# Kernel tuning notes

Measured on AMD Instinct MI355X. Metric: run time of the kernel, lower is better.

Reference implementation:

```python
import jax, jax.numpy as jnp
import numpy as np

HASH_BUCKETS = 1000
EMB_DIM = 16
LSTM_UNITS = 32
DENSE_UNITS = 32


def setup_inputs() -> dict:
    key = jax.random.key(0)
    ks = jax.random.split(key, 8)
    B, T = 4096, 512
    ids = jax.random.randint(ks[0], (B, T), 0, HASH_BUCKETS, dtype=jnp.int32)
    emb = jax.random.normal(ks[1], (HASH_BUCKETS, EMB_DIM), jnp.float32) * 0.05
    kernel = jax.random.normal(ks[2], (EMB_DIM, 4 * LSTM_UNITS), jnp.float32) * 0.1
    rec_kernel = jax.random.normal(ks[3], (LSTM_UNITS, 4 * LSTM_UNITS), jnp.float32) * 0.1
    w1 = jax.random.normal(ks[4], (LSTM_UNITS, DENSE_UNITS), jnp.float32) * 0.1
    b1 = jnp.zeros((DENSE_UNITS,), jnp.float32)
    w2 = jax.random.normal(ks[5], (DENSE_UNITS, 1), jnp.float32) * 0.1
    b2 = jnp.zeros((1,), jnp.float32)
    return {"ids": ids, "emb": emb, "kernel": kernel, "rec_kernel": rec_kernel,
            "w1": w1, "b1": b1, "w2": w2, "b2": b2}


def _lstm(x, kernel, rec_kernel):
    # x: [B, T, E]; Keras LSTM, use_bias=False, return last hidden state [B, H]
    B = x.shape[0]
    H = rec_kernel.shape[0]
    # precompute input projections for all timesteps: [T, B, 4H]
    xz = jnp.einsum('bte,ef->tbf', x, kernel)

    def step(carry, xz_t):
        h, c = carry
        z = xz_t + h @ rec_kernel  # [B, 4H]
        zi, zf, zc, zo = jnp.split(z, 4, axis=-1)  # Keras gate order i,f,c,o
        i = jax.nn.sigmoid(zi)
        f = jax.nn.sigmoid(zf)
        c = f * c + i * jnp.tanh(zc)
        o = jax.nn.sigmoid(zo)
        h = o * jnp.tanh(c)
        return (h, c), None

    init = (jnp.zeros((B, H), x.dtype), jnp.zeros((B, H), x.dtype))
    (h, _), _ = jax.lax.scan(step, init, xz)
    return h


def reference(ids, emb, kernel, rec_kernel, w1, b1, w2, b2):
    x = emb[ids]                        # [B, T, E] embedding lookup
    h = _lstm(x, kernel, rec_kernel)    # [B, H]
    y = jax.nn.relu(h @ w1 + b1)        # [B, 32]
    return y @ w2 + b2                  # [B, 1]
```

## Files before the change

### kernel.cpp

```cpp
#include <hip/hip_runtime.h>
#include <stdint.h>

#define HASH_BUCKETS 1000
#define EMB_DIM 16
#define HDIM 32
#define G4 128
#define TSTEPS 512
#define BATCH 4096

typedef short v8s __attribute__((ext_vector_type(8)));
typedef float v4f __attribute__((ext_vector_type(4)));

__device__ __forceinline__ float frcp(float x) {
    float r; asm("v_rcp_f32 %0, %1" : "=v"(r) : "v"(x)); return r;
}
__device__ __forceinline__ float fexp2(float x) {
    float r; asm("v_exp_f32 %0, %1" : "=v"(r) : "v"(x)); return r;
}
__device__ __forceinline__ uint32_t cvtpk_bf16(float lo, float hi) {
    uint32_t r; asm("v_cvt_pk_bf16_f32 %0, %1, %2" : "=v"(r) : "v"(lo), "v"(hi)); return r;
}
__device__ __forceinline__ uint32_t bf16rne(float x) {
    uint32_t u = __float_as_uint(x);
    return (u + 0x7FFFu + ((u >> 16) & 1u)) >> 16;
}

__global__ void precompute_P2_kernel(const float* __restrict__ emb,
                                     const float* __restrict__ kern,
                                     float* __restrict__ P2) {
    int idx = blockIdx.x * blockDim.x + threadIdx.x;
    if (idx >= HASH_BUCKETS * G4) return;
    int row = idx >> 7;
    int c2  = idx & 127;
    int h = c2 >> 2;
    int g = c2 & 3;
    float acc = 0.f;
#pragma unroll
    for (int e = 0; e < EMB_DIM; ++e)
        acc = fmaf(emb[row * EMB_DIM + e], kern[e * G4 + g * 32 + h], acc);
    float sg = (g == 2) ? 2.8853900817779268f : -1.4426950408889634f;
    P2[idx] = acc * sg;
}

__global__ __launch_bounds__(256)
__attribute__((amdgpu_waves_per_eu(1, 1)))
void lstm_head_kernel(const int* __restrict__ ids,
                      const float* __restrict__ P2,
                      const float* __restrict__ R,
                      const float* __restrict__ w1,
                      const float* __restrict__ b1,
                      const float* __restrict__ w2,
                      const float* __restrict__ b2,
                      float* __restrict__ out) {
    __shared__ __align__(16) uint32_t hbuf[2][16][36];
    __shared__ float hfin[16][33];

    const int tid  = threadIdx.x;
    const int w    = tid >> 6;
    const int lane = tid & 63;
    const int col  = lane & 15;
    const int quad = lane >> 4;
    const int bb   = blockIdx.x * 16;
    const int h0   = 8 * w + quad;
    const int h1   = h0 + 4;
    const int sw   = col & 3;

    const float PL2E   =  2.8853900817779268f;
    const float N2PL2E = -5.7707801635558536f;

    union V8 { uint32_t u[4]; v8s v; };
    V8 A0hi, A0lo, A1hi, A1lo;
    {
        int tt = col >> 2, g = col & 3;
        float sg = (g == 2) ? PL2E : -1.4426950408889634f;
        int gc0 = g * 32 + 8 * w + tt;
        int gc1 = gc0 + 4;
#pragma unroll
        for (int r = 0; r < 4; ++r) {
            uint32_t h0p[2], l0p[2], h1p[2], l1p[2];
#pragma unroll
            for (int e = 0; e < 2; ++e) {
                int k = quad * 8 + r + 4 * e;
                float x0 = R[k * G4 + gc0] * sg;
                uint32_t hb0 = bf16rne(x0);
                h0p[e] = hb0;
                l0p[e] = bf16rne(x0 - __uint_as_float(hb0 << 16));
                float x1 = R[k * G4 + gc1] * sg;
                uint32_t hb1 = bf16rne(x1);
                h1p[e] = hb1;
                l1p[e] = bf16rne(x1 - __uint_as_float(hb1 << 16));
            }
            A0hi.u[r] = h0p[0] | (h0p[1] << 16);
            A0lo.u[r] = l0p[0] | (l0p[1] << 16);
            A1hi.u[r] = h1p[0] | (h1p[1] << 16);
            A1lo.u[r] = l1p[0] | (l1p[1] << 16);
        }
    }

    for (int i = tid; i < 2 * 16 * 36; i += 256)
        ((uint32_t*)hbuf)[i] = 0u;

    const int* __restrict__ idrow = ids + (size_t)(bb + col) * TSTEPS;
    int ida = idrow[0];
    float4 xz0_c = *(const float4*)(P2 + (size_t)ida * G4 + 4 * h0);
    float4 xz1_c = *(const float4*)(P2 + (size_t)ida * G4 + 4 * h1);
    int idb = idrow[1];
    float4 xz0_n = *(const float4*)(P2 + (size_t)idb * G4 + 4 * h0);
    float4 xz1_n = *(const float4*)(P2 + (size_t)idb * G4 + 4 * h1);
    int id_c = idrow[2];
    int id_n = idrow[3];

    float c0 = 0.f, c1 = 0.f, hv0 = 0.f, hv1 = 0.f;
    const v4f vzero = {0.f, 0.f, 0.f, 0.f};

    const uint32_t* rdp[2] = { &hbuf[0][col][8 * (quad ^ sw)],
                               &hbuf[1][col][8 * (quad ^ sw)] };
    uint32_t* wrp[2] = { &hbuf[1][col][8 * (w ^ sw) + 2 * quad],
                         &hbuf[0][col][8 * (w ^ sw) + 2 * quad] };

    __syncthreads();

#define STEP(PB, T)                                                             \
    {                                                                           \
                  \
        uint4 dA = *(const uint4*)(rdp[PB]);                                    \
        uint4 dB = *(const uint4*)(rdp[PB] + 4);                                \
                      \
        float4 xz0_f = *(const float4*)(P2 + (size_t)id_c * G4 + 4 * h0);       \
        float4 xz1_f = *(const float4*)(P2 + (size_t)id_c * G4 + 4 * h1);       \
        int id_f = idrow[((T) + 4 < TSTEPS) ? ((T) + 4) : (TSTEPS - 1)];        \
        V8 Bhi, Blo;                                                            \
        Bhi.u[0] = __builtin_amdgcn_perm(dA.y, dA.x, 0x07060302u);              \
        Bhi.u[1] = __builtin_amdgcn_perm(dA.w, dA.z, 0x07060302u);              \
        Bhi.u[2] = __builtin_amdgcn_perm(dB.y, dB.x, 0x07060302u);              \
        Bhi.u[3] = __builtin_amdgcn_perm(dB.w, dB.z, 0x07060302u);              \
        Blo.u[0] = __builtin_amdgcn_perm(dA.y, dA.x, 0x05040100u);              \
        Blo.u[1] = __builtin_amdgcn_perm(dA.w, dA.z, 0x05040100u);              \
        Blo.u[2] = __builtin_amdgcn_perm(dB.y, dB.x, 0x05040100u);              \
        Blo.u[3] = __builtin_amdgcn_perm(dB.w, dB.z, 0x05040100u);              \
        v4f xzv0 = {xz0_c.x, xz0_c.y, xz0_c.z, xz0_c.w};                        \
        v4f xzv1 = {xz1_c.x, xz1_c.y, xz1_c.z, xz1_c.w};                        \
           \
        v4f m0a = __builtin_amdgcn_mfma_f32_16x16x32_bf16(A0lo.v, Bhi.v, vzero, 0, 0, 0); \
        v4f m0b = __builtin_amdgcn_mfma_f32_16x16x32_bf16(A0hi.v, Blo.v, vzero, 0, 0, 0); \
        v4f m0c = __builtin_amdgcn_mfma_f32_16x16x32_bf16(A0hi.v, Bhi.v, xzv0, 0, 0, 0);  \
        v4f m1a = __builtin_amdgcn_mfma_f32_16x16x32_bf16(A1lo.v, Bhi.v, vzero, 0, 0, 0); \
        v4f m1b = __builtin_amdgcn_mfma_f32_16x16x32_bf16(A1hi.v, Blo.v, vzero, 0, 0, 0); \
        v4f m1c = __builtin_amdgcn_mfma_f32_16x16x32_bf16(A1hi.v, Bhi.v, xzv1, 0, 0, 0);  \
        v4f z0 = (m0a + m0b) + m0c;                                             \
        v4f z1 = (m1a + m1b) + m1c;                                             \
                         \
        float di0 = 1.f + fexp2(z0[0]);                                         \
        float df0 = 1.f + fexp2(z0[1]);                                         \
        float dc0 = 1.f + fexp2(z0[2]);                                         \
        float dq0 = 1.f + fexp2(z0[3]);                                         \
        float di1 = 1.f + fexp2(z1[0]);                                         \
        float df1 = 1.f + fexp2(z1[1]);                                         \
        float dc1 = 1.f + fexp2(z1[2]);                                         \
        float dq1 = 1.f + fexp2(z1[3]);                                         \
        float Pp0 = di0 * df0, Qq0 = dc0 * dq0;                                 \
        float Pp1 = di1 * df1, Qq1 = dc1 * dq1;                                 \
        float rr0 = frcp(Pp0 * Qq0);                                            \
        float rr1 = frcp(Pp1 * Qq1);                                            \
        float rP0 = rr0 * Qq0, rQ0 = rr0 * Pp0;                                 \
        float rP1 = rr1 * Qq1, rQ1 = rr1 * Pp1;                                 \
        float ig0 = rP0 * df0, fg0 = rP0 * di0, rc0 = rQ0 * dq0, og0 = rQ0 * dc0; \
        float ig1 = rP1 * df1, fg1 = rP1 * di1, rc1 = rQ1 * dq1, og1 = rQ1 * dc1; \
        float tz0 = fmaf(N2PL2E, rc0, PL2E);                 \
        float tz1 = fmaf(N2PL2E, rc1, PL2E);                                    \
        c0 = fmaf(fg0, c0, ig0 * tz0);        \
        c1 = fmaf(fg1, c1, ig1 * tz1);                                          \
        float tc0 = fmaf(-2.f, frcp(1.f + fexp2(c0)), 1.f);                     \
        float tc1 = fmaf(-2.f, frcp(1.f + fexp2(c1)), 1.f);                     \
        hv0 = og0 * tc0;                                                        \
        hv1 = og1 * tc1;                                                        \
              \
        uint32_t t0 = cvtpk_bf16(hv0, hv0);                                     \
        float lo0 = hv0 - __uint_as_float(t0 & 0xffff0000u);                    \
        uint32_t pk0 = cvtpk_bf16(lo0, hv0);                                    \
        uint32_t t1 = cvtpk_bf16(hv1, hv1);                                     \
        float lo1 = hv1 - __uint_as_float(t1 & 0xffff0000u);                    \
        uint32_t pk1 = cvtpk_bf16(lo1, hv1);                                    \
        uint2 wv; wv.x = pk0; wv.y = pk1;                                       \
        *(uint2*)(wrp[PB]) = wv;   \
        xz0_c = xz0_n; xz1_c = xz1_n;                                           \
        xz0_n = xz0_f; xz1_n = xz1_f;                                           \
        id_c = id_n; id_n = id_f;                                               \
                                  \
        asm volatile("s_waitcnt lgkmcnt(0)\n\ts_barrier" ::: "memory");         \
    }

    for (int t = 0; t < TSTEPS; t += 2) {
        STEP(0, t)
        STEP(1, t + 1)
    }
#undef STEP

    hfin[col][h0] = hv0;
    hfin[col][h1] = hv1;
    __syncthreads();

    int u = tid & 31;
    for (int bq = tid >> 5; bq < 16; bq += 8) {
        float y = b1[u];
#pragma unroll
        for (int k = 0; k < HDIM; ++k)
            y = fmaf(hfin[bq][k], w1[k * HDIM + u], y);
        y = fmaxf(y, 0.f);
        float vv = y * w2[u];
#pragma unroll
        for (int off = 16; off >= 1; off >>= 1)
            vv += __shfl_xor(vv, off);
        if (u == 0) out[bb + bq] = vv + b2[0];
    }
}

extern "C" void kernel_launch(void* const* d_in, const int* in_sizes, int n_in,
                              void* d_out, int out_size, void* d_ws, size_t ws_size,
                              hipStream_t stream) {
    const int*   ids  = (const int*)d_in[0];
    const float* emb  = (const float*)d_in[1];
    const float* kern = (const float*)d_in[2];
    const float* rec  = (const float*)d_in[3];
    const float* w1   = (const float*)d_in[4];
    const float* b1   = (const float*)d_in[5];
    const float* w2   = (const float*)d_in[6];
    const float* b2   = (const float*)d_in[7];
    float* out = (float*)d_out;
    float* P2  = (float*)d_ws;

    precompute_P2_kernel<<<(HASH_BUCKETS * G4 + 255) / 256, 256, 0, stream>>>(
        emb, kern, P2);
    lstm_head_kernel<<<BATCH / 16, 256, 0, stream>>>(
        ids, P2, rec, w1, b1, w2, b2, out);
}
```

Baseline: 298.0 us.

## Split LSTM hidden units across eight waves with one unit per lane

Doubles the workgroup from 4 to 8 waves, so each lane computes one hidden unit instead of two. This halves the MFMA work and gate math per wave on the serial recurrence. The shared hidden-state buffer now stores separate hi/lo bf16 planes written as 16-bit stores, which removes the perm unpacking before the MFMA, and the swizzle and row stride change to match. In exchange, the per-step barrier now synchronizes 8 waves and the kernel allows 2 waves per EU. The extra sub-word stores may add LDS traffic.

```diff
diff --git a/kernel.cpp b/kernel.cpp
--- a/kernel.cpp
+++ b/kernel.cpp
@@ -7,6 +7,7 @@
 #define G4 128
 #define TSTEPS 512
 #define BATCH 4096
+#define RSTRIDE 40
 
 typedef short v8s __attribute__((ext_vector_type(8)));
 typedef float v4f __attribute__((ext_vector_type(4)));
@@ -17,8 +18,8 @@
 __device__ __forceinline__ float fexp2(float x) {
     float r; asm("v_exp_f32 %0, %1" : "=v"(r) : "v"(x)); return r;
 }
-__device__ __forceinline__ uint32_t cvtpk_bf16(float lo, float hi) {
-    uint32_t r; asm("v_cvt_pk_bf16_f32 %0, %1, %2" : "=v"(r) : "v"(lo), "v"(hi)); return r;
+__device__ __forceinline__ uint32_t cvtpk_bf16(float a, float b) {
+    uint32_t r; asm("v_cvt_pk_bf16_f32 %0, %1, %2" : "=v"(r) : "v"(a), "v"(b)); return r;
 }
 __device__ __forceinline__ uint32_t bf16rne(float x) {
     uint32_t u = __float_as_uint(x);
@@ -42,8 +43,8 @@
     P2[idx] = acc * sg;
 }
 
-__global__ __launch_bounds__(256)
-__attribute__((amdgpu_waves_per_eu(1, 1)))
+__global__ __launch_bounds__(512)
+__attribute__((amdgpu_waves_per_eu(2)))
 void lstm_head_kernel(const int* __restrict__ ids,
                       const float* __restrict__ P2,
                       const float* __restrict__ R,
@@ -52,7 +53,7 @@
                       const float* __restrict__ w2,
                       const float* __restrict__ b2,
                       float* __restrict__ out) {
-    __shared__ __align__(16) uint32_t hbuf[2][16][36];
+    __shared__ __align__(16) uint32_t hbuf[2][16][RSTRIDE];
     __shared__ float hfin[16][33];
 
     const int tid  = threadIdx.x;
@@ -61,132 +62,101 @@
     const int col  = lane & 15;
     const int quad = lane >> 4;
     const int bb   = blockIdx.x * 16;
-    const int h0   = 8 * w + quad;
-    const int h1   = h0 + 4;
-    const int sw   = col & 3;
+    const int unit = 4 * w + quad;
+    const int sw   = (col ^ (col >> 2)) & 3;
 
     const float PL2E   =  2.8853900817779268f;
+    const float NL2E   = -1.4426950408889634f;
     const float N2PL2E = -5.7707801635558536f;
 
     union V8 { uint32_t u[4]; v8s v; };
-    V8 A0hi, A0lo, A1hi, A1lo;
+    V8 Ahi, Alo;
     {
         int tt = col >> 2, g = col & 3;
-        float sg = (g == 2) ? PL2E : -1.4426950408889634f;
-        int gc0 = g * 32 + 8 * w + tt;
-        int gc1 = gc0 + 4;
+        float sg = (g == 2) ? PL2E : NL2E;
+        int gc = g * 32 + 4 * w + tt;
 #pragma unroll
         for (int r = 0; r < 4; ++r) {
-            uint32_t h0p[2], l0p[2], h1p[2], l1p[2];
+            uint32_t hp[2], lp[2];
 #pragma unroll
             for (int e = 0; e < 2; ++e) {
                 int k = quad * 8 + r + 4 * e;
-                float x0 = R[k * G4 + gc0] * sg;
-                uint32_t hb0 = bf16rne(x0);
-                h0p[e] = hb0;
-                l0p[e] = bf16rne(x0 - __uint_as_float(hb0 << 16));
-                float x1 = R[k * G4 + gc1] * sg;
-                uint32_t hb1 = bf16rne(x1);
-                h1p[e] = hb1;
-                l1p[e] = bf16rne(x1 - __uint_as_float(hb1 << 16));
+                float x = R[k * G4 + gc] * sg;
+                uint32_t hb = bf16rne(x);
+                hp[e] = hb;
+                lp[e] = bf16rne(x - __uint_as_float(hb << 16));
             }
-            A0hi.u[r] = h0p[0] | (h0p[1] << 16);
-            A0lo.u[r] = l0p[0] | (l0p[1] << 16);
-            A1hi.u[r] = h1p[0] | (h1p[1] << 16);
-            A1lo.u[r] = l1p[0] | (l1p[1] << 16);
+            Ahi.u[r] = hp[0] | (hp[1] << 16);
+            Alo.u[r] = lp[0] | (lp[1] << 16);
         }
     }
 
-    for (int i = tid; i < 2 * 16 * 36; i += 256)
+    for (int i = tid; i < 2 * 16 * RSTRIDE; i += 512)
         ((uint32_t*)hbuf)[i] = 0u;
+
+    const uint32_t* rdH[2] = { &hbuf[0][col][4 * (quad ^ sw)],
+                               &hbuf[1][col][4 * (quad ^ sw)] };
+    uint16_t* base16 = (uint16_t*)&hbuf[0][0][0];
+    const int bufhalf = 16 * RSTRIDE * 2;
+    {
+    }
+    const int hidw = col * RSTRIDE + 4 * (((w >> 1)) ^ sw) + quad;
+    const int h16  = hidw * 2 + (w & 1);
+    const int l16  = h16 + 32;
+    uint16_t* wrH[2] = { base16 + bufhalf + h16, base16 + h16 };
+    uint16_t* wrL[2] = { base16 + bufhalf + l16, base16 + l16 };
 
     const int* __restrict__ idrow = ids + (size_t)(bb + col) * TSTEPS;
     int ida = idrow[0];
-    float4 xz0_c = *(const float4*)(P2 + (size_t)ida * G4 + 4 * h0);
-    float4 xz1_c = *(const float4*)(P2 + (size_t)ida * G4 + 4 * h1);
+    float4 xz_c = *(const float4*)(P2 + (size_t)ida * G4 + 4 * unit);
     int idb = idrow[1];
-    float4 xz0_n = *(const float4*)(P2 + (size_t)idb * G4 + 4 * h0);
-    float4 xz1_n = *(const float4*)(P2 + (size_t)idb * G4 + 4 * h1);
+    float4 xz_n = *(const float4*)(P2 + (size_t)idb * G4 + 4 * unit);
     int id_c = idrow[2];
     int id_n = idrow[3];
 
-    float c0 = 0.f, c1 = 0.f, hv0 = 0.f, hv1 = 0.f;
+    float cc = 0.f, hv = 0.f;
     const v4f vzero = {0.f, 0.f, 0.f, 0.f};
 
-    const uint32_t* rdp[2] = { &hbuf[0][col][8 * (quad ^ sw)],
-                               &hbuf[1][col][8 * (quad ^ sw)] };
-    uint32_t* wrp[2] = { &hbuf[1][col][8 * (w ^ sw) + 2 * quad],
-                         &hbuf[0][col][8 * (w ^ sw) + 2 * quad] };
-
     __syncthreads();
+
+    union V8R { uint4 q; v8s v; };
 
 #define STEP(PB, T)                                                             \
     {                                                                           \
-                  \
-        uint4 dA = *(const uint4*)(rdp[PB]);                                    \
-        uint4 dB = *(const uint4*)(rdp[PB] + 4);                                \
-                      \
-        float4 xz0_f = *(const float4*)(P2 + (size_t)id_c * G4 + 4 * h0);       \
-        float4 xz1_f = *(const float4*)(P2 + (size_t)id_c * G4 + 4 * h1);       \
+                                  \
+        V8R Bhi, Blo;                                                           \
+        Bhi.q = *(const uint4*)(rdH[PB]);                                       \
+        Blo.q = *(const uint4*)(rdH[PB] + 16);                                  \
+                     \
+        float4 xz_f = *(const float4*)(P2 + (size_t)id_c * G4 + 4 * unit);      \
         int id_f = idrow[((T) + 4 < TSTEPS) ? ((T) + 4) : (TSTEPS - 1)];        \
-        V8 Bhi, Blo;                                                            \
-        Bhi.u[0] = __builtin_amdgcn_perm(dA.y, dA.x, 0x07060302u);              \
-        Bhi.u[1] = __builtin_amdgcn_perm(dA.w, dA.z, 0x07060302u);              \
-        Bhi.u[2] = __builtin_amdgcn_perm(dB.y, dB.x, 0x07060302u);              \
-        Bhi.u[3] = __builtin_amdgcn_perm(dB.w, dB.z, 0x07060302u);              \
-        Blo.u[0] = __builtin_amdgcn_perm(dA.y, dA.x, 0x05040100u);              \
-        Blo.u[1] = __builtin_amdgcn_perm(dA.w, dA.z, 0x05040100u);              \
-        Blo.u[2] = __builtin_amdgcn_perm(dB.y, dB.x, 0x05040100u);              \
-        Blo.u[3] = __builtin_amdgcn_perm(dB.w, dB.z, 0x05040100u);              \
-        v4f xzv0 = {xz0_c.x, xz0_c.y, xz0_c.z, xz0_c.w};                        \
-        v4f xzv1 = {xz1_c.x, xz1_c.y, xz1_c.z, xz1_c.w};                        \
-           \
-        v4f m0a = __builtin_amdgcn_mfma_f32_16x16x32_bf16(A0lo.v, Bhi.v, vzero, 0, 0, 0); \
-        v4f m0b = __builtin_amdgcn_mfma_f32_16x16x32_bf16(A0hi.v, Blo.v, vzero, 0, 0, 0); \
-        v4f m0c = __builtin_amdgcn_mfma_f32_16x16x32_bf16(A0hi.v, Bhi.v, xzv0, 0, 0, 0);  \
-        v4f m1a = __builtin_amdgcn_mfma_f32_16x16x32_bf16(A1lo.v, Bhi.v, vzero, 0, 0, 0); \
-        v4f m1b = __builtin_amdgcn_mfma_f32_16x16x32_bf16(A1hi.v, Blo.v, vzero, 0, 0, 0); \
-        v4f m1c = __builtin_amdgcn_mfma_f32_16x16x32_bf16(A1hi.v, Bhi.v, xzv1, 0, 0, 0);  \
-        v4f z0 = (m0a + m0b) + m0c;                                             \
-        v4f z1 = (m1a + m1b) + m1c;                                             \
-                         \
-        float di0 = 1.f + fexp2(z0[0]);                                         \
-        float df0 = 1.f + fexp2(z0[1]);                                         \
-        float dc0 = 1.f + fexp2(z0[2]);                                         \
-        float dq0 = 1.f + fexp2(z0[3]);                                         \
-        float di1 = 1.f + fexp2(z1[0]);                                         \
-        float df1 = 1.f + fexp2(z1[1]);                                         \
-        float dc1 = 1.f + fexp2(z1[2]);                                         \
-        float dq1 = 1.f + fexp2(z1[3]);                                         \
-        float Pp0 = di0 * df0, Qq0 = dc0 * dq0;                                 \
-        float Pp1 = di1 * df1, Qq1 = dc1 * dq1;                                 \
-        float rr0 = frcp(Pp0 * Qq0);                                            \
-        float rr1 = frcp(Pp1 * Qq1);                                            \
-        float rP0 = rr0 * Qq0, rQ0 = rr0 * Pp0;                                 \
-        float rP1 = rr1 * Qq1, rQ1 = rr1 * Pp1;                                 \
-        float ig0 = rP0 * df0, fg0 = rP0 * di0, rc0 = rQ0 * dq0, og0 = rQ0 * dc0; \
-        float ig1 = rP1 * df1, fg1 = rP1 * di1, rc1 = rQ1 * dq1, og1 = rQ1 * dc1; \
-        float tz0 = fmaf(N2PL2E, rc0, PL2E);                 \
-        float tz1 = fmaf(N2PL2E, rc1, PL2E);                                    \
-        c0 = fmaf(fg0, c0, ig0 * tz0);        \
-        c1 = fmaf(fg1, c1, ig1 * tz1);                                          \
-        float tc0 = fmaf(-2.f, frcp(1.f + fexp2(c0)), 1.f);                     \
-        float tc1 = fmaf(-2.f, frcp(1.f + fexp2(c1)), 1.f);                     \
-        hv0 = og0 * tc0;                                                        \
-        hv1 = og1 * tc1;                                                        \
-              \
-        uint32_t t0 = cvtpk_bf16(hv0, hv0);                                     \
-        float lo0 = hv0 - __uint_as_float(t0 & 0xffff0000u);                    \
-        uint32_t pk0 = cvtpk_bf16(lo0, hv0);                                    \
-        uint32_t t1 = cvtpk_bf16(hv1, hv1);                                     \
-        float lo1 = hv1 - __uint_as_float(t1 & 0xffff0000u);                    \
-        uint32_t pk1 = cvtpk_bf16(lo1, hv1);                                    \
-        uint2 wv; wv.x = pk0; wv.y = pk1;                                       \
-        *(uint2*)(wrp[PB]) = wv;   \
-        xz0_c = xz0_n; xz1_c = xz1_n;                                           \
-        xz0_n = xz0_f; xz1_n = xz1_f;                                           \
+        v4f xzv = {xz_c.x, xz_c.y, xz_c.z, xz_c.w};                             \
+        v4f ma = __builtin_amdgcn_mfma_f32_16x16x32_bf16(Alo.v, Bhi.v, vzero, 0, 0, 0); \
+        v4f mb = __builtin_amdgcn_mfma_f32_16x16x32_bf16(Ahi.v, Blo.v, vzero, 0, 0, 0); \
+        v4f mc = __builtin_amdgcn_mfma_f32_16x16x32_bf16(Ahi.v, Bhi.v, xzv, 0, 0, 0);   \
+        v4f z = (ma + mb) + mc;                                                 \
+                                               \
+        float di = 1.f + fexp2(z[0]);                                           \
+        float df = 1.f + fexp2(z[1]);                                           \
+        float dc = 1.f + fexp2(z[2]);                                           \
+        float dq = 1.f + fexp2(z[3]);                                           \
+        float Pp = di * df, Qq = dc * dq;                                       \
+        float rr = frcp(Pp * Qq);                                               \
+        float rP = rr * Qq, rQ = rr * Pp;                                       \
+        float ig = rP * df, fg = rP * di, rc = rQ * dq, og = rQ * dc;           \
+        float tz = fmaf(N2PL2E, rc, PL2E);                   \
+        cc = fmaf(fg, cc, ig * tz);                \
+        float tc = fmaf(-2.f, frcp(1.f + fexp2(cc)), 1.f);                      \
+        hv = og * tc;                                                           \
+                               \
+        uint32_t th = cvtpk_bf16(hv, hv);                                       \
+        wrH[PB][0] = (uint16_t)th;                                              \
+        float lo = hv - __uint_as_float(th << 16);                              \
+        uint32_t tl = cvtpk_bf16(lo, lo);                                       \
+        wrL[PB][0] = (uint16_t)tl;                                              \
+        xz_c = xz_n; xz_n = xz_f;                                               \
         id_c = id_n; id_n = id_f;                                               \
-                                  \
+                                               \
         asm volatile("s_waitcnt lgkmcnt(0)\n\ts_barrier" ::: "memory");         \
     }
 
@@ -196,12 +166,12 @@
     }
 #undef STEP
 
-    hfin[col][h0] = hv0;
-    hfin[col][h1] = hv1;
+    hfin[col][unit] = hv;
     __syncthreads();
 
-    int u = tid & 31;
-    for (int bq = tid >> 5; bq < 16; bq += 8) {
+    int u  = tid & 31;
+    int bq = tid >> 5;
+    {
         float y = b1[u];
 #pragma unroll
         for (int k = 0; k < HDIM; ++k)
@@ -231,6 +201,6 @@
 
     precompute_P2_kernel<<<(HASH_BUCKETS * G4 + 255) / 256, 256, 0, stream>>>(
         emb, kern, P2);
-    lstm_head_kernel<<<BATCH / 16, 256, 0, stream>>>(
+    lstm_head_kernel<<<BATCH / 16, 512, 0, stream>>>(
         ids, P2, rec, w1, b1, w2, b2, out);
 }
```

New measurement: 299.4 us. No clear change (+0.5%).

## Store hidden state as separate hi/lo bf16 planes to drop per-step permutes

Applied to the files above, without the earlier changes.

Changes the hidden-unit-to-lane mapping so each lane owns adjacent units, and writes the bf16 hi and lo parts of h into separate shared-memory planes. MFMA B operands then load directly without v_perm repacking, and one cvt_pk converts two units at once. The xz prefetch is restructured into even/odd register sets, and the P2 loads are moved to after the MFMA issue so they overlap. The XOR swizzle is removed, which may bring back LDS bank conflicts.

```diff
diff --git a/kernel.cpp b/kernel.cpp
--- a/kernel.cpp
+++ b/kernel.cpp
@@ -17,8 +17,8 @@
 __device__ __forceinline__ float fexp2(float x) {
     float r; asm("v_exp_f32 %0, %1" : "=v"(r) : "v"(x)); return r;
 }
-__device__ __forceinline__ uint32_t cvtpk_bf16(float lo, float hi) {
-    uint32_t r; asm("v_cvt_pk_bf16_f32 %0, %1, %2" : "=v"(r) : "v"(lo), "v"(hi)); return r;
+__device__ __forceinline__ uint32_t cvtpk_bf16(float a, float b) {
+    uint32_t r; asm("v_cvt_pk_bf16_f32 %0, %1, %2" : "=v"(r) : "v"(a), "v"(b)); return r;
 }
 __device__ __forceinline__ uint32_t bf16rne(float x) {
     uint32_t u = __float_as_uint(x);
@@ -61,26 +61,26 @@
     const int col  = lane & 15;
     const int quad = lane >> 4;
     const int bb   = blockIdx.x * 16;
-    const int h0   = 8 * w + quad;
-    const int h1   = h0 + 4;
-    const int sw   = col & 3;
+    const int u0   = 8 * w + 2 * quad;
+    const int u1   = u0 + 1;
 
     const float PL2E   =  2.8853900817779268f;
+    const float NL2E   = -1.4426950408889634f;
     const float N2PL2E = -5.7707801635558536f;
 
     union V8 { uint32_t u[4]; v8s v; };
     V8 A0hi, A0lo, A1hi, A1lo;
     {
         int tt = col >> 2, g = col & 3;
-        float sg = (g == 2) ? PL2E : -1.4426950408889634f;
-        int gc0 = g * 32 + 8 * w + tt;
-        int gc1 = gc0 + 4;
+        float sg = (g == 2) ? PL2E : NL2E;
+        int gc0 = g * 32 + 8 * w + 2 * tt;
+        int gc1 = gc0 + 1;
 #pragma unroll
         for (int r = 0; r < 4; ++r) {
             uint32_t h0p[2], l0p[2], h1p[2], l1p[2];
 #pragma unroll
             for (int e = 0; e < 2; ++e) {
-                int k = quad * 8 + r + 4 * e;
+                int k = quad * 8 + 2 * r + e;
                 float x0 = R[k * G4 + gc0] * sg;
                 uint32_t hb0 = bf16rne(x0);
                 h0p[e] = hb0;
@@ -100,56 +100,54 @@
     for (int i = tid; i < 2 * 16 * 36; i += 256)
         ((uint32_t*)hbuf)[i] = 0u;
 
+    const uint32_t* rd[2] = { &hbuf[0][col][4 * quad],
+                              &hbuf[1][col][4 * quad] };
+    uint32_t* wr[2] = { &hbuf[1][col][4 * w + quad],
+                        &hbuf[0][col][4 * w + quad] };
+
     const int* __restrict__ idrow = ids + (size_t)(bb + col) * TSTEPS;
-    int ida = idrow[0];
-    float4 xz0_c = *(const float4*)(P2 + (size_t)ida * G4 + 4 * h0);
-    float4 xz1_c = *(const float4*)(P2 + (size_t)ida * G4 + 4 * h1);
-    int idb = idrow[1];
-    float4 xz0_n = *(const float4*)(P2 + (size_t)idb * G4 + 4 * h0);
-    float4 xz1_n = *(const float4*)(P2 + (size_t)idb * G4 + 4 * h1);
-    int id_c = idrow[2];
-    int id_n = idrow[3];
+    const float* __restrict__ baseL = P2 + 4 * u0;
+    v4f xzE0, xzE1, xzO0, xzO1;
+    {
+        const float* p0 = baseL + (size_t)idrow[0] * G4;
+        const float* p1 = baseL + (size_t)idrow[1] * G4;
+        xzE0 = *(const v4f*)(p0);
+        xzE1 = *(const v4f*)(p0 + 4);
+        xzO0 = *(const v4f*)(p1);
+        xzO1 = *(const v4f*)(p1 + 4);
+    }
+    int idE = idrow[2];
+    int idO = idrow[3];
 
     float c0 = 0.f, c1 = 0.f, hv0 = 0.f, hv1 = 0.f;
     const v4f vzero = {0.f, 0.f, 0.f, 0.f};
 
-    const uint32_t* rdp[2] = { &hbuf[0][col][8 * (quad ^ sw)],
-                               &hbuf[1][col][8 * (quad ^ sw)] };
-    uint32_t* wrp[2] = { &hbuf[1][col][8 * (w ^ sw) + 2 * quad],
-                         &hbuf[0][col][8 * (w ^ sw) + 2 * quad] };
-
     __syncthreads();
 
-#define STEP(PB, T)                                                             \
+    union V8R { uint4 q; v8s v; };
+
+#define STEP(PB, XZ0, XZ1, IDX, T)                                              \
     {                                                                           \
-                  \
-        uint4 dA = *(const uint4*)(rdp[PB]);                                    \
-        uint4 dB = *(const uint4*)(rdp[PB] + 4);                                \
+             \
+        V8R Bhi, Blo;                                                           \
+        Bhi.q = *(const uint4*)(rd[PB]);                                        \
+        Blo.q = *(const uint4*)(rd[PB] + 16);                                   \
+        v4f ma0 = __builtin_amdgcn_mfma_f32_16x16x32_bf16(A0lo.v, Bhi.v, vzero, 0, 0, 0); \
+        v4f mb0 = __builtin_amdgcn_mfma_f32_16x16x32_bf16(A0hi.v, Blo.v, vzero, 0, 0, 0); \
+        v4f mc0 = __builtin_amdgcn_mfma_f32_16x16x32_bf16(A0hi.v, Bhi.v, XZ0, 0, 0, 0);   \
+        v4f ma1 = __builtin_amdgcn_mfma_f32_16x16x32_bf16(A1lo.v, Bhi.v, vzero, 0, 0, 0); \
+        v4f mb1 = __builtin_amdgcn_mfma_f32_16x16x32_bf16(A1hi.v, Blo.v, vzero, 0, 0, 0); \
+        v4f mc1 = __builtin_amdgcn_mfma_f32_16x16x32_bf16(A1hi.v, Bhi.v, XZ1, 0, 0, 0);   \
+            \
+        {                                                                       \
+            const float* pf_ = baseL + (size_t)(IDX) * G4;                      \
+            XZ0 = *(const v4f*)(pf_);                                           \
+            XZ1 = *(const v4f*)(pf_ + 4);                                       \
+        }                                                                       \
+        { int nt_ = (T) + 4; IDX = idrow[nt_ < TSTEPS ? nt_ : (TSTEPS - 1)]; }  \
+        v4f z0 = (ma0 + mb0) + mc0;                                             \
+        v4f z1 = (ma1 + mb1) + mc1;                                             \
                       \
-        float4 xz0_f = *(const float4*)(P2 + (size_t)id_c * G4 + 4 * h0);       \
-        float4 xz1_f = *(const float4*)(P2 + (size_t)id_c * G4 + 4 * h1);       \
-        int id_f = idrow[((T) + 4 < TSTEPS) ? ((T) + 4) : (TSTEPS - 1)];        \
-        V8 Bhi, Blo;                                                            \
-        Bhi.u[0] = __builtin_amdgcn_perm(dA.y, dA.x, 0x07060302u);              \
-        Bhi.u[1] = __builtin_amdgcn_perm(dA.w, dA.z, 0x07060302u);              \
-        Bhi.u[2] = __builtin_amdgcn_perm(dB.y, dB.x, 0x07060302u);              \
-        Bhi.u[3] = __builtin_amdgcn_perm(dB.w, dB.z, 0x07060302u);              \
-        Blo.u[0] = __builtin_amdgcn_perm(dA.y, dA.x, 0x05040100u);              \
-        Blo.u[1] = __builtin_amdgcn_perm(dA.w, dA.z, 0x05040100u);              \
-        Blo.u[2] = __builtin_amdgcn_perm(dB.y, dB.x, 0x05040100u);              \
-        Blo.u[3] = __builtin_amdgcn_perm(dB.w, dB.z, 0x05040100u);              \
-        v4f xzv0 = {xz0_c.x, xz0_c.y, xz0_c.z, xz0_c.w};                        \
-        v4f xzv1 = {xz1_c.x, xz1_c.y, xz1_c.z, xz1_c.w};                        \
-           \
-        v4f m0a = __builtin_amdgcn_mfma_f32_16x16x32_bf16(A0lo.v, Bhi.v, vzero, 0, 0, 0); \
-        v4f m0b = __builtin_amdgcn_mfma_f32_16x16x32_bf16(A0hi.v, Blo.v, vzero, 0, 0, 0); \
-        v4f m0c = __builtin_amdgcn_mfma_f32_16x16x32_bf16(A0hi.v, Bhi.v, xzv0, 0, 0, 0);  \
-        v4f m1a = __builtin_amdgcn_mfma_f32_16x16x32_bf16(A1lo.v, Bhi.v, vzero, 0, 0, 0); \
-        v4f m1b = __builtin_amdgcn_mfma_f32_16x16x32_bf16(A1hi.v, Blo.v, vzero, 0, 0, 0); \
-        v4f m1c = __builtin_amdgcn_mfma_f32_16x16x32_bf16(A1hi.v, Bhi.v, xzv1, 0, 0, 0);  \
-        v4f z0 = (m0a + m0b) + m0c;                                             \
-        v4f z1 = (m1a + m1b) + m1c;                                             \
-                         \
         float di0 = 1.f + fexp2(z0[0]);                                         \
         float df0 = 1.f + fexp2(z0[1]);                                         \
         float dc0 = 1.f + fexp2(z0[2]);                                         \
@@ -168,36 +166,30 @@
         float ig1 = rP1 * df1, fg1 = rP1 * di1, rc1 = rQ1 * dq1, og1 = rQ1 * dc1; \
         float tz0 = fmaf(N2PL2E, rc0, PL2E);                 \
         float tz1 = fmaf(N2PL2E, rc1, PL2E);                                    \
-        c0 = fmaf(fg0, c0, ig0 * tz0);        \
+        c0 = fmaf(fg0, c0, ig0 * tz0);             \
         c1 = fmaf(fg1, c1, ig1 * tz1);                                          \
         float tc0 = fmaf(-2.f, frcp(1.f + fexp2(c0)), 1.f);                     \
         float tc1 = fmaf(-2.f, frcp(1.f + fexp2(c1)), 1.f);                     \
         hv0 = og0 * tc0;                                                        \
         hv1 = og1 * tc1;                                                        \
-              \
-        uint32_t t0 = cvtpk_bf16(hv0, hv0);                                     \
-        float lo0 = hv0 - __uint_as_float(t0 & 0xffff0000u);                    \
-        uint32_t pk0 = cvtpk_bf16(lo0, hv0);                                    \
-        uint32_t t1 = cvtpk_bf16(hv1, hv1);                                     \
-        float lo1 = hv1 - __uint_as_float(t1 & 0xffff0000u);                    \
-        uint32_t pk1 = cvtpk_bf16(lo1, hv1);                                    \
-        uint2 wv; wv.x = pk0; wv.y = pk1;                                       \
-        *(uint2*)(wrp[PB]) = wv;   \
-        xz0_c = xz0_n; xz1_c = xz1_n;                                           \
-        xz0_n = xz0_f; xz1_n = xz1_f;                                           \
-        id_c = id_n; id_n = id_f;                                               \
-                                  \
+                       \
+        uint32_t ph = cvtpk_bf16(hv0, hv1);                                     \
+        wr[PB][0] = ph;                                                         \
+        float lo0 = hv0 - __uint_as_float(ph << 16);                            \
+        float lo1 = hv1 - __uint_as_float(ph & 0xffff0000u);                    \
+        wr[PB][16] = cvtpk_bf16(lo0, lo1);                                      \
+                     \
         asm volatile("s_waitcnt lgkmcnt(0)\n\ts_barrier" ::: "memory");         \
     }
 
     for (int t = 0; t < TSTEPS; t += 2) {
-        STEP(0, t)
-        STEP(1, t + 1)
+        STEP(0, xzE0, xzE1, idE, t)
+        STEP(1, xzO0, xzO1, idO, t + 1)
     }
 #undef STEP
 
-    hfin[col][h0] = hv0;
-    hfin[col][h1] = hv1;
+    hfin[col][u0] = hv0;
+    hfin[col][u1] = hv1;
     __syncthreads();
 
     int u = tid & 31;
```

Result: faster. 242.2 us (-18.7%).
